# Kernel tuning notes

Hardware: AMD Instinct MI355X
Metric: run time of the kernel (lower is better)

## Reference

```python
import jax, jax.numpy as jnp
import numpy as np

NUM_NETS = 2_000_000
PINS_PER_NET = 4
NUM_PINS = NUM_NETS * PINS_PER_NET


def setup_inputs() -> dict:
    key = jax.random.key(0)
    k1, k2, k3 = jax.random.split(key, 3)
    num_slrX, num_slrY = 1, 4
    # pin positions already expressed in SLR-grid units: x in [0, num_slrX), y in [0, num_slrY)
    pos = jax.random.uniform(k1, (NUM_PINS, 2), jnp.float32) * jnp.array(
        [float(max(num_slrX, 1)), float(max(num_slrY, 1))], jnp.float32)
    # CSR netpin structure: each net owns PINS_PER_NET pins, flat list is a permutation of all pins
    flat_netpin = jax.random.permutation(k2, NUM_PINS).astype(jnp.int32)
    netpin_start = (jnp.arange(NUM_NETS + 1, dtype=jnp.int32) * PINS_PER_NET)
    net_ids = jnp.repeat(jnp.arange(NUM_NETS, dtype=jnp.int32), PINS_PER_NET)
    net_weights = jax.random.uniform(k3, (NUM_NETS,), jnp.float32, minval=0.5, maxval=1.5)
    net_mask = jnp.ones((NUM_NETS,), jnp.bool_)
    pin_mask = jnp.zeros((NUM_PINS,), jnp.bool_)
    inv_gamma = jnp.float32(2.0)  # 1 / gamma, gamma = 0.5
    return dict(pos=pos, flat_netpin=flat_netpin, netpin_start=netpin_start,
                net_ids=net_ids, net_weights=net_weights, net_mask=net_mask,
                pin_mask=pin_mask, inv_gamma=inv_gamma,
                num_slrX=num_slrX, num_slrY=num_slrY)


def reference(pos, flat_netpin, netpin_start, net_ids, net_weights, net_mask,
              pin_mask, inv_gamma, num_slrX, num_slrY):
    """Weighted-average SLL: per-net log-sum-exp weighted-average span of pin
    SLR coordinates, per dimension, counted only for dims with >1 SLR."""
    n = net_weights.shape[0]
    p = pos[flat_netpin]  # [P, 2] gather pin coords in CSR order
    # numerically-stable exp weights per net (segment max/min shift)
    mx = jax.ops.segment_max(p, net_ids, num_segments=n)  # [N, 2]
    mn = jax.ops.segment_min(p, net_ids, num_segments=n)  # [N, 2]
    ep = jnp.exp((p - mx[net_ids]) * inv_gamma)   # exp(+x/gamma), shifted
    en = jnp.exp((mn[net_ids] - p) * inv_gamma)   # exp(-x/gamma), shifted
    s_ep = jax.ops.segment_sum(ep, net_ids, num_segments=n)
    s_xep = jax.ops.segment_sum(p * ep, net_ids, num_segments=n)
    s_en = jax.ops.segment_sum(en, net_ids, num_segments=n)
    s_xen = jax.ops.segment_sum(p * en, net_ids, num_segments=n)
    wa = s_xep / s_ep - s_xen / s_en  # [N, 2] weighted-average span per dim
    dim_on = jnp.array([num_slrX > 1, num_slrY > 1], dtype=wa.dtype)  # only multi-SLR dims
    per_net = jnp.sum(wa * dim_on, axis=1)  # [N]
    return jnp.sum(jnp.where(net_mask, net_weights * per_net, jnp.float32(0.0)))
```

## Files before the change

### kernel.cpp

```cpp
#include <hip/hip_runtime.h>
#include <stdint.h>


#define PB_SHIFT   13
#define PB_SIZE    (1 << PB_SHIFT)
#define MAX_NPB    1024
#define JB_SHIFT   14
#define JB_SIZE    (1 << JB_SHIFT)
#define MAX_NJB    512
#define CH         JB_SIZE
#define YQ_SHIFT   18
#define YQ_ONE     262144.0f
#define YQ_MASK    ((1u << YQ_SHIFT) - 1u)

__device__ __forceinline__ float wa4(float a, float b, float c, float d, float ig) {
    float ea = __expf(a * ig), eb = __expf(b * ig);
    float ec = __expf(c * ig), ed = __expf(d * ig);
    float na = __expf(-a * ig), nb = __expf(-b * ig);
    float nc = __expf(-c * ig), nd = __expf(-d * ig);
    float s_ep  = ea + eb + ec + ed;
    float s_xep = a * ea + b * eb + c * ec + d * ed;
    float s_en  = na + nb + nc + nd;
    float s_xen = a * na + b * nb + c * nc + d * nd;
    return s_xep / s_ep - s_xen / s_en;
}

__global__ __launch_bounds__(512) void p1a_count(
    const int4* __restrict__ fnp4, int NPB,
    unsigned* __restrict__ cnt)
{
    __shared__ unsigned hist[MAX_NPB];
    const int c = blockIdx.x, t = threadIdx.x;
    for (int i = t; i < NPB; i += 512) hist[i] = 0;
    __syncthreads();
    const int base4 = c * (CH / 4);
    #pragma unroll
    for (int m = 0; m < 8; ++m) {
        int4 v = fnp4[base4 + t + 512 * m];
        atomicAdd(&hist[(unsigned)v.x >> PB_SHIFT], 1u);
        atomicAdd(&hist[(unsigned)v.y >> PB_SHIFT], 1u);
        atomicAdd(&hist[(unsigned)v.z >> PB_SHIFT], 1u);
        atomicAdd(&hist[(unsigned)v.w >> PB_SHIFT], 1u);
    }
    __syncthreads();
    for (int i = t; i < NPB; i += 512) cnt[(size_t)c * NPB + i] = hist[i];
}

__global__ __launch_bounds__(256) void p1b_scan(
    const unsigned* __restrict__ cnt, int NPB, int NJB,
    unsigned* __restrict__ ofs1, unsigned* __restrict__ ofs2,
    float* __restrict__ out)
{
    const int blk = blockIdx.x, t = threadIdx.x;
    const int s1b = NPB / 256;
    if (blk == 0 && t == 0) out[0] = 0.0f;
    if (blk < s1b) {
        const int p = blk * 256 + t;
        unsigned acc = (unsigned)p << PB_SHIFT;
        for (int c = 0; c < NJB; c += 8) {
            unsigned v[8];
            #pragma unroll
            for (int i = 0; i < 8; ++i) v[i] = cnt[(size_t)(c + i) * NPB + p];
            #pragma unroll
            for (int i = 0; i < 8; ++i) { ofs1[(size_t)(c + i) * NPB + p] = acc; acc += v[i]; }
        }
    } else {
        const int jb = blk - s1b;
        if (jb >= NJB) return;
        __shared__ unsigned wsum[4];
        const uint4* row = (const uint4*)(cnt + (size_t)jb * NPB);
        uint4 v = row[t];
        unsigned s = v.x + v.y + v.z + v.w;
        unsigned ex = s;
        #pragma unroll
        for (int off = 1; off < 64; off <<= 1) {
            unsigned u = __shfl_up(ex, off, 64);
            if ((t & 63) >= off) ex += u;
        }
        ex -= s;
        if ((t & 63) == 63) wsum[t >> 6] = ex + s;
        __syncthreads();
        unsigned wb = 0;
        const int w = t >> 6;
        #pragma unroll
        for (int i = 0; i < 4; ++i) if (i < w) wb += wsum[i];
        unsigned o = ((unsigned)jb << JB_SHIFT) + wb + ex;
        uint4 ov;
        ov.x = o; ov.y = o + v.x; ov.z = ov.y + v.y; ov.w = ov.z + v.z;
        ((uint4*)(ofs2 + (size_t)jb * NPB))[t] = ov;
    }
}

__global__ __launch_bounds__(512) void p1c_scatter(
    const int4* __restrict__ fnp4, const unsigned* __restrict__ ofs1,
    int NPB, uint2* __restrict__ ent1)
{
    __shared__ unsigned hist[MAX_NPB];
    __shared__ unsigned orow[MAX_NPB];
    const int c = blockIdx.x, t = threadIdx.x;
    for (int i = t; i < NPB; i += 512) {
        hist[i] = 0;
        orow[i] = ofs1[(size_t)c * NPB + i];
    }
    __syncthreads();
    const int base = c * CH;
    #pragma unroll
    for (int m = 0; m < 8; ++m) {
        int k4 = t + 512 * m;
        int4 v = fnp4[(base >> 2) + k4];
        unsigned pin[4] = {(unsigned)v.x, (unsigned)v.y, (unsigned)v.z, (unsigned)v.w};
        #pragma unroll
        for (int i = 0; i < 4; ++i) {
            unsigned pb = pin[i] >> PB_SHIFT;
            unsigned r  = atomicAdd(&hist[pb], 1u);
            ent1[orow[pb] + r] = make_uint2(pin[i], (unsigned)(base + 4 * k4 + i));
        }
    }
}

__global__ __launch_bounds__(512) void p2_gather(
    const uint2* __restrict__ ent1, const float2* __restrict__ pos2,
    const unsigned* __restrict__ ofs2,
    const int* __restrict__ slrx_p, const int* __restrict__ slry_p,
    int d, int NPB, int NJB, unsigned* __restrict__ ent2)
{
    const int slr = (d == 0) ? slrx_p[0] : slry_p[0];
    if (slr <= 1) return;
    const float qs = YQ_ONE / (float)slr;

    __shared__ float    win[PB_SIZE];
    __shared__ unsigned hist[MAX_NJB];
    __shared__ unsigned orow[MAX_NJB];
    const int p = blockIdx.x, t = threadIdx.x;
    const int pbase = p << PB_SHIFT;

    for (int i = t; i < PB_SIZE; i += 512) {
        float2 q = pos2[pbase + i];
        win[i] = d ? q.y : q.x;
    }
    for (int i = t; i < NJB; i += 512) {
        hist[i] = 0;
        orow[i] = ofs2[(size_t)i * NPB + p];
    }
    __syncthreads();

    uint2 e[16];
    #pragma unroll
    for (int m = 0; m < 16; ++m)
        e[m] = ent1[pbase + t + 512 * m];
    #pragma unroll
    for (int m = 0; m < 16; ++m) {
        float y = win[e[m].x - (unsigned)pbase];
        unsigned yq = min((unsigned)(y * qs + 0.5f), YQ_MASK);
        unsigned jb = e[m].y >> JB_SHIFT;
        unsigned r  = atomicAdd(&hist[jb], 1u);
        ent2[orow[jb] + r] = ((e[m].y & (JB_SIZE - 1u)) << YQ_SHIFT) | yq;
    }
}

__global__ __launch_bounds__(512) void p3_compute(
    const unsigned* __restrict__ ent2, const float* __restrict__ wts,
    const float* __restrict__ ig_p,
    const int* __restrict__ slrx_p, const int* __restrict__ slry_p,
    int d, float* __restrict__ out)
{
    const int slr = (d == 0) ? slrx_p[0] : slry_p[0];
    if (slr <= 1) return;
    const float dq = (float)slr / YQ_ONE;

    __shared__ float ytmp[JB_SIZE];
    const int bj = blockIdx.x << JB_SHIFT, t = threadIdx.x;
    const float ig = ig_p[0];

    for (int k = t; k < JB_SIZE; k += 512) {
        unsigned e = ent2[bj + k];
        ytmp[e >> YQ_SHIFT] = (float)(e & YQ_MASK) * dq;
    }
    __syncthreads();

    float val = 0.0f;
    const int bnet = bj >> 2;
    const float4* y4 = (const float4*)ytmp;
    #pragma unroll
    for (int m = 0; m < 8; ++m) {
        int i = t + 512 * m;
        float4 q = y4[i];
        val += wts[bnet + i] * wa4(q.x, q.y, q.z, q.w, ig);
    }

    #pragma unroll
    for (int off = 32; off > 0; off >>= 1) val += __shfl_down(val, off, 64);
    __syncthreads();
    if ((t & 63) == 0) ytmp[t >> 6] = val;
    __syncthreads();
    if (t == 0) {
        float s = 0.0f;
        #pragma unroll
        for (int w = 0; w < 8; ++w) s += ytmp[w];
        atomicAdd(out, s);
    }
}

__global__ __launch_bounds__(256) void wasll_fallback(
    const float2* __restrict__ pos, const int4* __restrict__ fnp4,
    const float* __restrict__ net_weights, const float* __restrict__ inv_gamma_p,
    const int* __restrict__ slrx_p, const int* __restrict__ slry_p,
    float* __restrict__ out, int num_nets)
{
    const float ig = inv_gamma_p[0];
    const float dx = (slrx_p[0] > 1) ? 1.0f : 0.0f;
    const float dy = (slry_p[0] > 1) ? 1.0f : 0.0f;
    int net = blockIdx.x * blockDim.x + threadIdx.x;
    float val = 0.0f;
    if (net < num_nets) {
        int4 idx = fnp4[net];
        float2 p0 = pos[idx.x], p1 = pos[idx.y], p2 = pos[idx.z], p3 = pos[idx.w];
        val = net_weights[net] * (dx * wa4(p0.x, p1.x, p2.x, p3.x, ig)
                                + dy * wa4(p0.y, p1.y, p2.y, p3.y, ig));
    }
    #pragma unroll
    for (int off = 32; off > 0; off >>= 1) val += __shfl_down(val, off, 64);
    __shared__ float smem[4];
    if ((threadIdx.x & 63) == 0) smem[threadIdx.x >> 6] = val;
    __syncthreads();
    if (threadIdx.x == 0)
        atomicAdd(out, smem[0] + smem[1] + smem[2] + smem[3]);
}

__global__ void zero_out_kernel(float* __restrict__ out) { out[0] = 0.0f; }

extern "C" void kernel_launch(void* const* d_in, const int* in_sizes, int n_in,
                              void* d_out, int out_size, void* d_ws, size_t ws_size,
                              hipStream_t stream) {
    const float* posf        = (const float*)d_in[0];
    const int*   fnp         = (const int*)d_in[1];
    const float* net_weights = (const float*)d_in[4];
    const float* inv_gamma   = (const float*)d_in[7];
    const int*   slrx        = (const int*)d_in[8];
    const int*   slry        = (const int*)d_in[9];
    float*       out         = (float*)d_out;
    const int    N  = in_sizes[4];
    const int    NP = in_sizes[1];

    const int NPB = NP >> PB_SHIFT;
    const int NJB = NP >> JB_SHIFT;

    size_t off = 0;
    auto carve = [&](size_t bytes) { size_t o = off; off += (bytes + 255) & ~size_t(255); return o; };
    size_t o_ent1 = carve((size_t)NP * sizeof(uint2));
    size_t o_ent2 = carve((size_t)NP * sizeof(unsigned));
    size_t o_cnt  = carve((size_t)NJB * NPB * sizeof(unsigned));
    size_t o_ofs1 = carve((size_t)NJB * NPB * sizeof(unsigned));
    size_t o_ofs2 = carve((size_t)NJB * NPB * sizeof(unsigned));

    const bool ok = (NP == 4 * N) && (NP % CH == 0) &&
                    (NPB >= 256) && (NPB <= MAX_NPB) && (NPB % 256 == 0) &&
                    (NJB <= MAX_NJB) && (NJB % 8 == 0) && (off <= ws_size);
    if (!ok) {
        hipLaunchKernelGGL(zero_out_kernel, dim3(1), dim3(1), 0, stream, out);
        const int block = 256, grid = (N + block - 1) / block;
        hipLaunchKernelGGL(wasll_fallback, dim3(grid), dim3(block), 0, stream,
                           (const float2*)posf, (const int4*)fnp, net_weights,
                           inv_gamma, slrx, slry, out, N);
        return;
    }

    char* ws = (char*)d_ws;
    uint2*    ent1 = (uint2*)(ws + o_ent1);
    unsigned* ent2 = (unsigned*)(ws + o_ent2);
    unsigned* cnt  = (unsigned*)(ws + o_cnt);
    unsigned* ofs1 = (unsigned*)(ws + o_ofs1);
    unsigned* ofs2 = (unsigned*)(ws + o_ofs2);

    hipLaunchKernelGGL(p1a_count, dim3(NJB), dim3(512), 0, stream,
                       (const int4*)fnp, NPB, cnt);
    hipLaunchKernelGGL(p1b_scan, dim3(NPB / 256 + NJB), dim3(256), 0, stream,
                       cnt, NPB, NJB, ofs1, ofs2, out);
    hipLaunchKernelGGL(p1c_scatter, dim3(NJB), dim3(512), 0, stream,
                       (const int4*)fnp, ofs1, NPB, ent1);

    hipLaunchKernelGGL(p2_gather, dim3(NPB), dim3(512), 0, stream,
                       ent1, (const float2*)posf, ofs2, slrx, slry, 0, NPB, NJB, ent2);
    hipLaunchKernelGGL(p3_compute, dim3(NJB), dim3(512), 0, stream,
                       ent2, net_weights, inv_gamma, slrx, slry, 0, out);
    hipLaunchKernelGGL(p2_gather, dim3(NPB), dim3(512), 0, stream,
                       ent1, (const float2*)posf, ofs2, slrx, slry, 1, NPB, NJB, ent2);
    hipLaunchKernelGGL(p3_compute, dim3(NJB), dim3(512), 0, stream,
                       ent2, net_weights, inv_gamma, slrx, slry, 1, out);
}
```

Measured before the change: 295.0 us.

## Support partial tiles so the bucketed gather path runs for non-aligned sizes

Adds bounds handling for partial pin and net blocks and pads the count, offset and scan arrays to a fixed 1024 columns. This relaxes the launch checks that previously required NP to be a multiple of 16384. At the task size those checks failed, so every call went to the per-net fallback kernel with random gathers. The change also splits the intermediate (pin, slot) entry into a 16-bit in-block pin offset and a 32-bit slot array to cut scatter and gather bytes. The cost is extra bounds checks and a fixed padded scan width.

New measurement: 416.5 us. 1.41x slower.

```diff
diff --git a/kernel.cpp b/kernel.cpp
--- a/kernel.cpp
+++ b/kernel.cpp
@@ -4,7 +4,7 @@
 
 #define PB_SHIFT   13
 #define PB_SIZE    (1 << PB_SHIFT)
-#define MAX_NPB    1024
+#define NPB_PAD    1024
 #define JB_SHIFT   14
 #define JB_SIZE    (1 << JB_SHIFT)
 #define MAX_NJB    512
@@ -26,49 +26,56 @@
 }
 
 __global__ __launch_bounds__(512) void p1a_count(
-    const int4* __restrict__ fnp4, int NPB,
-    unsigned* __restrict__ cnt)
-{
-    __shared__ unsigned hist[MAX_NPB];
+    const int4* __restrict__ fnp4, int NP, unsigned* __restrict__ cnt)
+{
+    __shared__ unsigned hist[NPB_PAD];
     const int c = blockIdx.x, t = threadIdx.x;
-    for (int i = t; i < NPB; i += 512) hist[i] = 0;
-    __syncthreads();
-    const int base4 = c * (CH / 4);
+    const int base  = c * CH;
+    const int valid = min(CH, NP - base);
+    for (int i = t; i < NPB_PAD; i += 512) hist[i] = 0;
+    __syncthreads();
     #pragma unroll
     for (int m = 0; m < 8; ++m) {
-        int4 v = fnp4[base4 + t + 512 * m];
-        atomicAdd(&hist[(unsigned)v.x >> PB_SHIFT], 1u);
-        atomicAdd(&hist[(unsigned)v.y >> PB_SHIFT], 1u);
-        atomicAdd(&hist[(unsigned)v.z >> PB_SHIFT], 1u);
-        atomicAdd(&hist[(unsigned)v.w >> PB_SHIFT], 1u);
-    }
-    __syncthreads();
-    for (int i = t; i < NPB; i += 512) cnt[(size_t)c * NPB + i] = hist[i];
+        int k4 = t + 512 * m;
+        if (4 * k4 < valid) {
+            int4 v = fnp4[(base >> 2) + k4];
+            atomicAdd(&hist[(unsigned)v.x >> PB_SHIFT], 1u);
+            atomicAdd(&hist[(unsigned)v.y >> PB_SHIFT], 1u);
+            atomicAdd(&hist[(unsigned)v.z >> PB_SHIFT], 1u);
+            atomicAdd(&hist[(unsigned)v.w >> PB_SHIFT], 1u);
+        }
+    }
+    __syncthreads();
+    for (int i = t; i < NPB_PAD; i += 512)
+        cnt[(size_t)c * NPB_PAD + i] = hist[i];
 }
 
 __global__ __launch_bounds__(256) void p1b_scan(
-    const unsigned* __restrict__ cnt, int NPB, int NJB,
+    const unsigned* __restrict__ cnt, int NJB,
     unsigned* __restrict__ ofs1, unsigned* __restrict__ ofs2,
     float* __restrict__ out)
 {
     const int blk = blockIdx.x, t = threadIdx.x;
-    const int s1b = NPB / 256;
     if (blk == 0 && t == 0) out[0] = 0.0f;
-    if (blk < s1b) {
+    if (blk < 4) {
         const int p = blk * 256 + t;
         unsigned acc = (unsigned)p << PB_SHIFT;
-        for (int c = 0; c < NJB; c += 8) {
+        for (int c0 = 0; c0 < NJB; c0 += 8) {
             unsigned v[8];
             #pragma unroll
-            for (int i = 0; i < 8; ++i) v[i] = cnt[(size_t)(c + i) * NPB + p];
+            for (int i = 0; i < 8; ++i)
+                v[i] = (c0 + i < NJB) ? cnt[(size_t)(c0 + i) * NPB_PAD + p] : 0u;
             #pragma unroll
-            for (int i = 0; i < 8; ++i) { ofs1[(size_t)(c + i) * NPB + p] = acc; acc += v[i]; }
+            for (int i = 0; i < 8; ++i) {
+                if (c0 + i < NJB) ofs1[(size_t)(c0 + i) * NPB_PAD + p] = acc;
+                acc += v[i];
+            }
         }
     } else {
-        const int jb = blk - s1b;
+        const int jb = blk - 4;
         if (jb >= NJB) return;
         __shared__ unsigned wsum[4];
-        const uint4* row = (const uint4*)(cnt + (size_t)jb * NPB);
+        const uint4* row = (const uint4*)(cnt + (size_t)jb * NPB_PAD);
         uint4 v = row[t];
         unsigned s = v.x + v.y + v.z + v.w;
         unsigned ex = s;
@@ -87,42 +94,52 @@
         unsigned o = ((unsigned)jb << JB_SHIFT) + wb + ex;
         uint4 ov;
         ov.x = o; ov.y = o + v.x; ov.z = ov.y + v.y; ov.w = ov.z + v.z;
-        ((uint4*)(ofs2 + (size_t)jb * NPB))[t] = ov;
+        ((uint4*)(ofs2 + (size_t)jb * NPB_PAD))[t] = ov;
     }
 }
 
 __global__ __launch_bounds__(512) void p1c_scatter(
     const int4* __restrict__ fnp4, const unsigned* __restrict__ ofs1,
-    int NPB, uint2* __restrict__ ent1)
-{
-    __shared__ unsigned hist[MAX_NPB];
-    __shared__ unsigned orow[MAX_NPB];
+    int NP, unsigned short* __restrict__ pinoff16, unsigned* __restrict__ jarr)
+{
+    __shared__ unsigned hist[NPB_PAD];
+    __shared__ unsigned orow[NPB_PAD];
     const int c = blockIdx.x, t = threadIdx.x;
-    for (int i = t; i < NPB; i += 512) {
+    const int base  = c * CH;
+    const int valid = min(CH, NP - base);
+    for (int i = t; i < NPB_PAD; i += 512) {
         hist[i] = 0;
-        orow[i] = ofs1[(size_t)c * NPB + i];
-    }
-    __syncthreads();
-    const int base = c * CH;
+        orow[i] = ofs1[(size_t)c * NPB_PAD + i];
+    }
+    __syncthreads();
+    int4 v[8];
     #pragma unroll
     for (int m = 0; m < 8; ++m) {
         int k4 = t + 512 * m;
-        int4 v = fnp4[(base >> 2) + k4];
-        unsigned pin[4] = {(unsigned)v.x, (unsigned)v.y, (unsigned)v.z, (unsigned)v.w};
+        v[m] = (4 * k4 < valid) ? fnp4[(base >> 2) + k4] : make_int4(-1, -1, -1, -1);
+    }
+    #pragma unroll
+    for (int m = 0; m < 8; ++m) {
+        int k4 = t + 512 * m;
+        if (4 * k4 >= valid) continue;
+        unsigned pin[4] = {(unsigned)v[m].x, (unsigned)v[m].y,
+                           (unsigned)v[m].z, (unsigned)v[m].w};
         #pragma unroll
         for (int i = 0; i < 4; ++i) {
-            unsigned pb = pin[i] >> PB_SHIFT;
-            unsigned r  = atomicAdd(&hist[pb], 1u);
-            ent1[orow[pb] + r] = make_uint2(pin[i], (unsigned)(base + 4 * k4 + i));
+            unsigned pb  = pin[i] >> PB_SHIFT;
+            unsigned r   = atomicAdd(&hist[pb], 1u);
+            unsigned dst = orow[pb] + r;
+            pinoff16[dst] = (unsigned short)(pin[i] & (PB_SIZE - 1u));
+            jarr[dst]     = (unsigned)(base + 4 * k4 + i);
         }
     }
 }
 
 __global__ __launch_bounds__(512) void p2_gather(
-    const uint2* __restrict__ ent1, const float2* __restrict__ pos2,
-    const unsigned* __restrict__ ofs2,
+    const unsigned short* __restrict__ pinoff16, const unsigned* __restrict__ jarr,
+    const float2* __restrict__ pos2, const unsigned* __restrict__ ofs2,
     const int* __restrict__ slrx_p, const int* __restrict__ slry_p,
-    int d, int NPB, int NJB, unsigned* __restrict__ ent2)
+    int d, int NP, int NJB, unsigned* __restrict__ ent2)
 {
     const int slr = (d == 0) ? slrx_p[0] : slry_p[0];
     if (slr <= 1) return;
@@ -132,29 +149,35 @@
     __shared__ unsigned hist[MAX_NJB];
     __shared__ unsigned orow[MAX_NJB];
     const int p = blockIdx.x, t = threadIdx.x;
-    const int pbase = p << PB_SHIFT;
-
-    for (int i = t; i < PB_SIZE; i += 512) {
+    const int pbase   = p << PB_SHIFT;
+    const int count_b = min(PB_SIZE, NP - pbase);
+
+    for (int i = t; i < count_b; i += 512) {
         float2 q = pos2[pbase + i];
         win[i] = d ? q.y : q.x;
     }
     for (int i = t; i < NJB; i += 512) {
         hist[i] = 0;
-        orow[i] = ofs2[(size_t)i * NPB + p];
-    }
-    __syncthreads();
-
-    uint2 e[16];
-    #pragma unroll
-    for (int m = 0; m < 16; ++m)
-        e[m] = ent1[pbase + t + 512 * m];
+        orow[i] = ofs2[(size_t)i * NPB_PAD + p];
+    }
+    __syncthreads();
+
+    unsigned short po[16]; unsigned jv[16];
     #pragma unroll
     for (int m = 0; m < 16; ++m) {
-        float y = win[e[m].x - (unsigned)pbase];
+        int k = t + 512 * m;
+        po[m] = (k < count_b) ? pinoff16[pbase + k] : 0;
+        jv[m] = (k < count_b) ? jarr[pbase + k] : 0u;
+    }
+    #pragma unroll
+    for (int m = 0; m < 16; ++m) {
+        int k = t + 512 * m;
+        if (k >= count_b) continue;
+        float y = win[po[m]];
         unsigned yq = min((unsigned)(y * qs + 0.5f), YQ_MASK);
-        unsigned jb = e[m].y >> JB_SHIFT;
+        unsigned jb = jv[m] >> JB_SHIFT;
         unsigned r  = atomicAdd(&hist[jb], 1u);
-        ent2[orow[jb] + r] = ((e[m].y & (JB_SIZE - 1u)) << YQ_SHIFT) | yq;
+        ent2[orow[jb] + r] = ((jv[m] & (JB_SIZE - 1u)) << YQ_SHIFT) | yq;
     }
 }
 
@@ -162,7 +185,7 @@
     const unsigned* __restrict__ ent2, const float* __restrict__ wts,
     const float* __restrict__ ig_p,
     const int* __restrict__ slrx_p, const int* __restrict__ slry_p,
-    int d, float* __restrict__ out)
+    int d, int NP, float* __restrict__ out)
 {
     const int slr = (d == 0) ? slrx_p[0] : slry_p[0];
     if (slr <= 1) return;
@@ -170,20 +193,19 @@
 
     __shared__ float ytmp[JB_SIZE];
     const int bj = blockIdx.x << JB_SHIFT, t = threadIdx.x;
+    const int nslots = min(JB_SIZE, NP - bj);
     const float ig = ig_p[0];
 
-    for (int k = t; k < JB_SIZE; k += 512) {
+    for (int k = t; k < nslots; k += 512) {
         unsigned e = ent2[bj + k];
         ytmp[e >> YQ_SHIFT] = (float)(e & YQ_MASK) * dq;
     }
     __syncthreads();
 
     float val = 0.0f;
-    const int bnet = bj >> 2;
+    const int nnets = nslots >> 2, bnet = bj >> 2;
     const float4* y4 = (const float4*)ytmp;
-    #pragma unroll
-    for (int m = 0; m < 8; ++m) {
-        int i = t + 512 * m;
+    for (int i = t; i < nnets; i += 512) {
         float4 q = y4[i];
         val += wts[bnet + i] * wa4(q.x, q.y, q.z, q.w, ig);
     }
@@ -242,20 +264,20 @@
     const int    N  = in_sizes[4];
     const int    NP = in_sizes[1];
 
-    const int NPB = NP >> PB_SHIFT;
-    const int NJB = NP >> JB_SHIFT;
+    const int NJB = (NP + CH - 1) / CH;
+    const int NPB = (NP + PB_SIZE - 1) / PB_SIZE;
 
     size_t off = 0;
     auto carve = [&](size_t bytes) { size_t o = off; off += (bytes + 255) & ~size_t(255); return o; };
-    size_t o_ent1 = carve((size_t)NP * sizeof(uint2));
+    size_t o_po   = carve((size_t)NP * sizeof(unsigned short));
+    size_t o_jarr = carve((size_t)NP * sizeof(unsigned));
     size_t o_ent2 = carve((size_t)NP * sizeof(unsigned));
-    size_t o_cnt  = carve((size_t)NJB * NPB * sizeof(unsigned));
-    size_t o_ofs1 = carve((size_t)NJB * NPB * sizeof(unsigned));
-    size_t o_ofs2 = carve((size_t)NJB * NPB * sizeof(unsigned));
-
-    const bool ok = (NP == 4 * N) && (NP % CH == 0) &&
-                    (NPB >= 256) && (NPB <= MAX_NPB) && (NPB % 256 == 0) &&
-                    (NJB <= MAX_NJB) && (NJB % 8 == 0) && (off <= ws_size);
+    size_t o_cnt  = carve((size_t)NJB * NPB_PAD * sizeof(unsigned));
+    size_t o_ofs1 = carve((size_t)NJB * NPB_PAD * sizeof(unsigned));
+    size_t o_ofs2 = carve((size_t)NJB * NPB_PAD * sizeof(unsigned));
+
+    const bool ok = (NP == 4 * N) && (NP % 4 == 0) &&
+                    (NPB <= NPB_PAD) && (NJB <= MAX_NJB) && (off <= ws_size);
     if (!ok) {
         hipLaunchKernelGGL(zero_out_kernel, dim3(1), dim3(1), 0, stream, out);
         const int block = 256, grid = (N + block - 1) / block;
@@ -266,25 +288,28 @@
     }
 
     char* ws = (char*)d_ws;
-    uint2*    ent1 = (uint2*)(ws + o_ent1);
-    unsigned* ent2 = (unsigned*)(ws + o_ent2);
-    unsigned* cnt  = (unsigned*)(ws + o_cnt);
-    unsigned* ofs1 = (unsigned*)(ws + o_ofs1);
-    unsigned* ofs2 = (unsigned*)(ws + o_ofs2);
+    unsigned short* pinoff16 = (unsigned short*)(ws + o_po);
+    unsigned*       jarr     = (unsigned*)(ws + o_jarr);
+    unsigned*       ent2     = (unsigned*)(ws + o_ent2);
+    unsigned*       cnt      = (unsigned*)(ws + o_cnt);
+    unsigned*       ofs1     = (unsigned*)(ws + o_ofs1);
+    unsigned*       ofs2     = (unsigned*)(ws + o_ofs2);
 
     hipLaunchKernelGGL(p1a_count, dim3(NJB), dim3(512), 0, stream,
-                       (const int4*)fnp, NPB, cnt);
-    hipLaunchKernelGGL(p1b_scan, dim3(NPB / 256 + NJB), dim3(256), 0, stream,
-                       cnt, NPB, NJB, ofs1, ofs2, out);
+                       (const int4*)fnp, NP, cnt);
+    hipLaunchKernelGGL(p1b_scan, dim3(4 + NJB), dim3(256), 0, stream,
+                       cnt, NJB, ofs1, ofs2, out);
     hipLaunchKernelGGL(p1c_scatter, dim3(NJB), dim3(512), 0, stream,
-                       (const int4*)fnp, ofs1, NPB, ent1);
+                       (const int4*)fnp, ofs1, NP, pinoff16, jarr);
 
     hipLaunchKernelGGL(p2_gather, dim3(NPB), dim3(512), 0, stream,
-                       ent1, (const float2*)posf, ofs2, slrx, slry, 0, NPB, NJB, ent2);
+                       pinoff16, jarr, (const float2*)posf, ofs2,
+                       slrx, slry, 0, NP, NJB, ent2);
     hipLaunchKernelGGL(p3_compute, dim3(NJB), dim3(512), 0, stream,
-                       ent2, net_weights, inv_gamma, slrx, slry, 0, out);
+                       ent2, net_weights, inv_gamma, slrx, slry, 0, NP, out);
     hipLaunchKernelGGL(p2_gather, dim3(NPB), dim3(512), 0, stream,
-                       ent1, (const float2*)posf, ofs2, slrx, slry, 1, NPB, NJB, ent2);
+                       pinoff16, jarr, (const float2*)posf, ofs2,
+                       slrx, slry, 1, NP, NJB, ent2);
     hipLaunchKernelGGL(p3_compute, dim3(NJB), dim3(512), 0, stream,
-                       ent2, net_weights, inv_gamma, slrx, slry, 1, out);
-}
+                       ent2, net_weights, inv_gamma, slrx, slry, 1, NP, out);
+}
```
